# Kernel optimization log

Measured on AMD Instinct MI355X. Metric: run time of the kernel, lower is better.

Reference implementation:

```python
import jax, jax.numpy as jnp
import numpy as np

DIM = 512
NUM_HEADS = 8
HEAD_DIM = DIM // NUM_HEADS
SCALE = HEAD_DIM ** -0.5


def setup_inputs() -> dict:
    key = jax.random.key(0)
    ks = jax.random.split(key, 6)
    B, N, C = 2, 4096, DIM
    s = C ** -0.5  # init scale, torch Linear default-ish
    return {
        "x": jax.random.normal(ks[0], (B, N, C), dtype=jnp.float32),
        "Wq": jax.random.normal(ks[1], (C, C), dtype=jnp.float32) * s,
        "Wk": jax.random.normal(ks[2], (C, C), dtype=jnp.float32) * s,
        "Wv": jax.random.normal(ks[3], (C, C), dtype=jnp.float32) * s,
        "Wo": jax.random.normal(ks[4], (C, C), dtype=jnp.float32) * s,
        "bo": jax.random.normal(ks[5], (C,), dtype=jnp.float32) * s,
    }


def reference(x, Wq, Wk, Wv, Wo, bo):
    B, N, C = x.shape
    H, D = NUM_HEADS, HEAD_DIM
    # torch nn.Linear: y = x @ W.T
    q = (x @ Wq.T).reshape(B, N, H, D).transpose(0, 2, 1, 3)  # [B,H,N,D]
    k = (x @ Wk.T).reshape(B, N, H, D).transpose(0, 2, 1, 3)
    v = (x @ Wv.T).reshape(B, N, H, D).transpose(0, 2, 1, 3)
    attn = jnp.einsum("bhnd,bhmd->bhnm", q, k) * SCALE  # [B,H,N,N]
    attn = jax.nn.softmax(attn, axis=-1)
    out = jnp.einsum("bhnm,bhmd->bhnd", attn, v)
    out = out.transpose(0, 2, 1, 3).reshape(B, N, C)
    return out @ Wo.T + bo
```

## Files before the change

### kernel.cpp

```cpp
#include <hip/hip_runtime.h>
#include <hip/hip_bf16.h>
#include <cstdint>
#include <cstddef>

using bf16 = __bf16;
typedef __attribute__((ext_vector_type(8))) __bf16 bf16x8;
typedef __attribute__((ext_vector_type(4))) float  f32x4;

#define LOG2E 1.4426950408889634f

__device__ inline void gld_lds16(const void* g, void* l) {
  __builtin_amdgcn_global_load_lds(
      (const __attribute__((address_space(1))) void*)g,
      (__attribute__((address_space(3))) void*)l, 16, 0, 0);
}

__global__ __launch_bounds__(256) void k_cvt_all(
    const float* __restrict__ x, const float* __restrict__ wq,
    const float* __restrict__ wk, const float* __restrict__ wv,
    const float* __restrict__ wo, bf16* __restrict__ xb,
    bf16* __restrict__ wqkv, bf16* __restrict__ wob) {
  int i = blockIdx.x * 256 + threadIdx.x;
  const float* s;
  bf16* d;
  int local;
  if (i < 524288) {
    s = x; d = xb; local = i;
  } else {
    int i2 = i - 524288;
    int which = i2 >> 15;
    local = i2 & 32767;
    s = (which == 0) ? wq : (which == 1) ? wk : (which == 2) ? wv : wo;
    d = (which < 3) ? (wqkv + ((size_t)which << 18)) : wob;
  }
  const float4* p = ((const float4*)s) + (size_t)local * 2;
  float4 a = p[0], b = p[1];
  bf16x8 o;
  o[0] = (bf16)a.x; o[1] = (bf16)a.y; o[2] = (bf16)a.z; o[3] = (bf16)a.w;
  o[4] = (bf16)b.x; o[5] = (bf16)b.y; o[6] = (bf16)b.z; o[7] = (bf16)b.w;
  *(bf16x8*)(d + (size_t)local * 8) = o;
}

__global__ __launch_bounds__(256) void k_gemm(
    const bf16* __restrict__ A, const bf16* __restrict__ B, int mode,
    bf16* __restrict__ Qb, bf16* __restrict__ Kb, bf16* __restrict__ Vtb,
    float* __restrict__ outf, const float* __restrict__ bias) {
  const int K = 512;
  __shared__ alignas(16) bf16 As[128 * 64];
  __shared__ alignas(16) bf16 Bs[128 * 64];
  const int tid = threadIdx.x;
  const int wave = tid >> 6, lane = tid & 63;
  const int l15 = lane & 15, l4 = lane >> 4;
  const int m0 = blockIdx.x * 128, n0 = blockIdx.y * 128;
  const int wr = wave >> 1, wc = wave & 1;
  f32x4 acc[4][4] = {};

  for (int k0 = 0; k0 < K; k0 += 64) {
#pragma unroll
    for (int it = 0; it < 4; ++it) {
      int c = it * 256 + tid;
      int row = c >> 3, kc = c & 7;
      int sb = (kc * 16) ^ ((row & 7) << 4);
      gld_lds16((const char*)A + ((size_t)(m0 + row) * K + k0) * 2 + sb,
                (char*)As + c * 16);
      gld_lds16((const char*)B + ((size_t)(n0 + row) * K + k0) * 2 + sb,
                (char*)Bs + c * 16);
    }
    __syncthreads();
#pragma unroll
    for (int ks = 0; ks < 2; ++ks) {
      bf16x8 af[4], bff[4];
#pragma unroll
      for (int mf = 0; mf < 4; ++mf) {
        int r = wr * 64 + mf * 16 + l15;
        af[mf] = *(const bf16x8*)((const char*)As + r * 128 +
                                  ((ks * 64 + l4 * 16) ^ ((r & 7) << 4)));
      }
#pragma unroll
      for (int nf = 0; nf < 4; ++nf) {
        int r = wc * 64 + nf * 16 + l15;
        bff[nf] = *(const bf16x8*)((const char*)Bs + r * 128 +
                                   ((ks * 64 + l4 * 16) ^ ((r & 7) << 4)));
      }
#pragma unroll
      for (int mf = 0; mf < 4; ++mf)
#pragma unroll
        for (int nf = 0; nf < 4; ++nf)
          acc[mf][nf] = __builtin_amdgcn_mfma_f32_16x16x32_bf16(
              af[mf], bff[nf], acc[mf][nf], 0, 0, 0);
    }
    __syncthreads();
  }

#pragma unroll
  for (int mf = 0; mf < 4; ++mf)
#pragma unroll
    for (int nf = 0; nf < 4; ++nf)
#pragma unroll
      for (int r = 0; r < 4; ++r) {
        int m = m0 + wr * 64 + mf * 16 + l4 * 4 + r;
        int n = n0 + wc * 64 + nf * 16 + l15;
        float v = acc[mf][nf][r];
        if (mode == 1) {
          outf[(size_t)m * 512 + n] = v + bias[n];
        } else {
          int which = n >> 9, o = n & 511, h = o >> 6, d = o & 63;
          int b = m >> 12, nr = m & 4095;
          if (which == 0)
            Qb[((size_t)(b * 8 + h) * 4096 + nr) * 64 + d] = (bf16)(v * 0.125f);
          else if (which == 1)
            Kb[((size_t)(b * 8 + h) * 4096 + nr) * 64 + d] = (bf16)v;
          else
            Vtb[((size_t)((b * 8 + h) * 64 + d)) * 4096 + nr] = (bf16)v;
        }
      }
}

template <int NS>
__global__ __launch_bounds__(256, 4) void k_attn_t(
    const bf16* __restrict__ Q, const bf16* __restrict__ Kg,
    const bf16* __restrict__ Vt, bf16* __restrict__ AO,
    float* __restrict__ pO, float* __restrict__ pD) {
  __shared__ alignas(16) bf16 Ks[64 * 64];
  __shared__ alignas(16) bf16 Vs[64 * 64];
  __shared__ alignas(16) bf16 Ps[4][32 * 64];
  const int tid = threadIdx.x, wave = tid >> 6, lane = tid & 63;
  const int l15 = lane & 15, l4 = lane >> 4;
  const int bh = blockIdx.y, q0 = blockIdx.x * 128;
  const int z = (NS > 1) ? blockIdx.z : 0;
  const int n_lo = z * (4096 / NS);
  const int NT = 4096 / NS / 64;
  const char* Qb = (const char*)(Q + (size_t)bh * 4096 * 64);
  const char* Kb = (const char*)(Kg + (size_t)bh * 4096 * 64);
  const char* Vb = (const char*)(Vt + (size_t)bh * 64 * 4096);

  const int c0 = tid, c1 = 256 + tid;
  const int row0 = c0 >> 3, sb0 = ((c0 & 7) * 16) ^ ((row0 & 7) << 4);
  const int row1 = c1 >> 3, sb1 = ((c1 & 7) * 16) ^ ((row1 & 7) << 4);
  const char* ksrc0 = Kb + (size_t)(n_lo + row0) * 128 + sb0;
  const char* ksrc1 = Kb + (size_t)(n_lo + row1) * 128 + sb1;
  const char* vsrc0 = Vb + (size_t)row0 * 8192 + (size_t)n_lo * 2 + sb0;
  const char* vsrc1 = Vb + (size_t)row1 * 8192 + (size_t)n_lo * 2 + sb1;
  char* kdst0 = (char*)Ks + c0 * 16;
  char* kdst1 = (char*)Ks + c1 * 16;
  char* vdst0 = (char*)Vs + c0 * 16;
  char* vdst1 = (char*)Vs + c1 * 16;

  const char* kf_p[2][4];
#pragma unroll
  for (int cf = 0; cf < 4; ++cf) {
    int kv = cf * 16 + l15;
#pragma unroll
    for (int ds = 0; ds < 2; ++ds)
      kf_p[ds][cf] = (const char*)Ks + kv * 128 +
                     ((ds * 64 + l4 * 16) ^ ((kv & 7) << 4));
  }
  const char* vf_p[4][2];
#pragma unroll
  for (int df = 0; df < 4; ++df) {
    int d = df * 16 + l15;
#pragma unroll
    for (int ks = 0; ks < 2; ++ks)
      vf_p[df][ks] = (const char*)Vs + d * 128 +
                     ((ks * 64 + l4 * 16) ^ ((d & 7) << 4));
  }
  char* pw_p[4][4];
#pragma unroll
  for (int r = 0; r < 4; ++r) {
    int q = l4 * 4 + r;
#pragma unroll
    for (int cf = 0; cf < 4; ++cf)
      pw_p[r][cf] = (char*)Ps[wave] + q * 128 +
                    (((cf * 16 + l15) * 2) ^ ((q & 7) << 4));
  }
  const char* pf_p[2];
#pragma unroll
  for (int ks = 0; ks < 2; ++ks)
    pf_p[ks] = (const char*)Ps[wave] + l15 * 128 +
               ((ks * 64 + l4 * 16) ^ ((l15 & 7) << 4));

  bf16x8 qf[2][2];
#pragma unroll
  for (int mrow = 0; mrow < 2; ++mrow)
#pragma unroll
    for (int ds = 0; ds < 2; ++ds)
      qf[mrow][ds] = *(const bf16x8*)(Qb +
          ((size_t)(q0 + wave * 32 + mrow * 16 + l15) * 64 + ds * 32 + l4 * 8) * 2);

  bf16x8 vone;
#pragma unroll
  for (int j = 0; j < 8; ++j) vone[j] = (bf16)1.0f;

  f32x4 oacc[2][4] = {};
  f32x4 dacc[2] = {};

  for (int t = 0; t < NT; ++t) {
    gld_lds16(ksrc0, kdst0);
    gld_lds16(vsrc0, vdst0);
    gld_lds16(ksrc1, kdst1);
    gld_lds16(vsrc1, vdst1);
    ksrc0 += 8192; ksrc1 += 8192;
    vsrc0 += 128;  vsrc1 += 128;
    __syncthreads();

    f32x4 s[2][4];
#pragma unroll
    for (int cf = 0; cf < 4; ++cf) {
      bf16x8 kf0 = *(const bf16x8*)kf_p[0][cf];
      bf16x8 kf1 = *(const bf16x8*)kf_p[1][cf];
#pragma unroll
      for (int mrow = 0; mrow < 2; ++mrow) {
        f32x4 z2 = {};
        z2 = __builtin_amdgcn_mfma_f32_16x16x32_bf16(qf[mrow][0], kf0, z2, 0, 0, 0);
        z2 = __builtin_amdgcn_mfma_f32_16x16x32_bf16(qf[mrow][1], kf1, z2, 0, 0, 0);
        s[mrow][cf] = z2;
      }
    }

#pragma unroll
    for (int mrow = 0; mrow < 2; ++mrow)
#pragma unroll
      for (int r = 0; r < 4; ++r)
#pragma unroll
        for (int cf = 0; cf < 4; ++cf) {
          float p = __builtin_amdgcn_exp2f(s[mrow][cf][r] * LOG2E);
          *(bf16*)(pw_p[r][cf] + mrow * 2048) = (bf16)p;
        }

    bf16x8 pf[2][2];
#pragma unroll
    for (int mrow = 0; mrow < 2; ++mrow) {
      pf[mrow][0] = *(const bf16x8*)(pf_p[0] + mrow * 2048);
      pf[mrow][1] = *(const bf16x8*)(pf_p[1] + mrow * 2048);
    }

#pragma unroll
    for (int mrow = 0; mrow < 2; ++mrow) {
      dacc[mrow] = __builtin_amdgcn_mfma_f32_16x16x32_bf16(pf[mrow][0], vone,
                                                           dacc[mrow], 0, 0, 0);
      dacc[mrow] = __builtin_amdgcn_mfma_f32_16x16x32_bf16(pf[mrow][1], vone,
                                                           dacc[mrow], 0, 0, 0);
    }

#pragma unroll
    for (int df = 0; df < 4; ++df) {
      bf16x8 vf0 = *(const bf16x8*)vf_p[df][0];
      bf16x8 vf1 = *(const bf16x8*)vf_p[df][1];
#pragma unroll
      for (int mrow = 0; mrow < 2; ++mrow) {
        oacc[mrow][df] = __builtin_amdgcn_mfma_f32_16x16x32_bf16(
            pf[mrow][0], vf0, oacc[mrow][df], 0, 0, 0);
        oacc[mrow][df] = __builtin_amdgcn_mfma_f32_16x16x32_bf16(
            pf[mrow][1], vf1, oacc[mrow][df], 0, 0, 0);
      }
    }
    __syncthreads();
  }

  if (NS > 1) {
    float* po = pO + (((size_t)(z * 16 + bh)) * 4096) * 64;
    float* pd = pD + ((size_t)(z * 16 + bh)) * 4096;
#pragma unroll
    for (int mrow = 0; mrow < 2; ++mrow)
#pragma unroll
      for (int r = 0; r < 4; ++r) {
        int n = q0 + wave * 32 + mrow * 16 + l4 * 4 + r;
#pragma unroll
        for (int df = 0; df < 4; ++df)
          po[(size_t)n * 64 + df * 16 + l15] = oacc[mrow][df][r];
        if (l15 == 0) pd[n] = dacc[mrow][r];
      }
  } else {
    int b = bh >> 3, h = bh & 7;
#pragma unroll
    for (int mrow = 0; mrow < 2; ++mrow)
#pragma unroll
      for (int r = 0; r < 4; ++r) {
        float inv = 1.0f / dacc[mrow][r];
        int n = q0 + wave * 32 + mrow * 16 + l4 * 4 + r;
#pragma unroll
        for (int df = 0; df < 4; ++df) {
          int d = df * 16 + l15;
          AO[((size_t)(b * 4096 + n)) * 512 + h * 64 + d] =
              (bf16)(oacc[mrow][df][r] * inv);
        }
      }
  }
}

__global__ __launch_bounds__(256) void k_comb(
    const float* __restrict__ pO, const float* __restrict__ pD,
    bf16* __restrict__ AO) {
  const size_t SO = (size_t)16 * 4096 * 64;
  const size_t SD = (size_t)16 * 4096;
  int i = blockIdx.x * 256 + threadIdx.x;
  int g = i >> 3, j = i & 7;
  float den = pD[g] + pD[g + SD];
  float inv = 1.0f / den;
  const float* a = pO + (size_t)g * 64 + j * 8;
  const float* b2 = a + SO;
  bf16x8 o;
#pragma unroll
  for (int t = 0; t < 8; ++t) o[t] = (bf16)((a[t] + b2[t]) * inv);
  int bh = g >> 12, n = g & 4095, b = bh >> 3, h = bh & 7;
  *(bf16x8*)(AO + ((size_t)(b * 4096 + n)) * 512 + h * 64 + j * 8) = o;
}

extern "C" void kernel_launch(void* const* d_in, const int* in_sizes, int n_in,
                              void* d_out, int out_size, void* d_ws,
                              size_t ws_size, hipStream_t stream) {
  const float* x  = (const float*)d_in[0];
  const float* Wq = (const float*)d_in[1];
  const float* Wk = (const float*)d_in[2];
  const float* Wv = (const float*)d_in[3];
  const float* Wo = (const float*)d_in[4];
  const float* bo = (const float*)d_in[5];
  float* out = (float*)d_out;

  char* ws = (char*)d_ws;
  bf16* xb   = (bf16*)(ws);
  bf16* wqkv = (bf16*)(ws + (8u << 20));
  bf16* wob  = (bf16*)(ws + (8u << 20) + 1572864u);
  bf16* Qb   = (bf16*)(ws + (10u << 20));
  bf16* Kb   = (bf16*)(ws + (18u << 20));
  bf16* Vtb  = (bf16*)(ws + (26u << 20));
  bf16* AOb  = (bf16*)(ws + (34u << 20));
  float* pD  = (float*)(ws + (42u << 20));
  float* pO  = (float*)(ws + (43u << 20));

  k_cvt_all<<<2560, 256, 0, stream>>>(x, Wq, Wk, Wv, Wo, xb, wqkv, wob);

  k_gemm<<<dim3(64, 12), 256, 0, stream>>>(xb, wqkv, 0, Qb, Kb, Vtb,
                                           nullptr, nullptr);

  if (ws_size >= ((size_t)75 << 20)) {
    k_attn_t<2><<<dim3(32, 16, 2), 256, 0, stream>>>(Qb, Kb, Vtb, nullptr,
                                                     pO, pD);
    k_comb<<<2048, 256, 0, stream>>>(pO, pD, AOb);
  } else {
    k_attn_t<1><<<dim3(32, 16), 256, 0, stream>>>(Qb, Kb, Vtb, AOb,
                                                  nullptr, nullptr);
  }

  k_gemm<<<dim3(64, 4), 256, 0, stream>>>(AOb, wob, 1, nullptr, nullptr,
                                          nullptr, out, bo);
}
```

Measured before the change: 161.2 us.

## Double-buffer K/V LDS tiles in attention kernel to overlap loads with compute

Doubles the shared-memory K and V tiles and restructures the attention loop into a ping-pong pipeline. The next tile's global-to-LDS loads are issued before computing on the current buffer. The aim is to hide global load latency behind the MFMA and exp work. In exchange, LDS use per block rises from about 32KB to 48KB, which may lower occupancy at 4 blocks per CU. The code also assumes NT is even, and the loop relies on the barrier placement to keep the ping-pong buffers correct.

```diff
diff --git a/kernel.cpp b/kernel.cpp
--- a/kernel.cpp
+++ b/kernel.cpp
@@ -121,8 +121,8 @@
     const bf16* __restrict__ Q, const bf16* __restrict__ Kg,
     const bf16* __restrict__ Vt, bf16* __restrict__ AO,
     float* __restrict__ pO, float* __restrict__ pD) {
-  __shared__ alignas(16) bf16 Ks[64 * 64];
-  __shared__ alignas(16) bf16 Vs[64 * 64];
+  __shared__ alignas(16) bf16 Ks[2][64 * 64];
+  __shared__ alignas(16) bf16 Vs[2][64 * 64];
   __shared__ alignas(16) bf16 Ps[4][32 * 64];
   const int tid = threadIdx.x, wave = tid >> 6, lane = tid & 63;
   const int l15 = lane & 15, l4 = lane >> 4;
@@ -194,68 +194,83 @@
   f32x4 oacc[2][4] = {};
   f32x4 dacc[2] = {};
 
-  for (int t = 0; t < NT; ++t) {
-    gld_lds16(ksrc0, kdst0);
-    gld_lds16(vsrc0, vdst0);
-    gld_lds16(ksrc1, kdst1);
-    gld_lds16(vsrc1, vdst1);
-    ksrc0 += 8192; ksrc1 += 8192;
-    vsrc0 += 128;  vsrc1 += 128;
+#define STAGE(BO)                                                             \
+  do {                                                                        \
+    gld_lds16(ksrc0, kdst0 + (BO));                                           \
+    gld_lds16(vsrc0, vdst0 + (BO));                                           \
+    gld_lds16(ksrc1, kdst1 + (BO));                                           \
+    gld_lds16(vsrc1, vdst1 + (BO));                                           \
+    ksrc0 += 8192; ksrc1 += 8192;                                             \
+    vsrc0 += 128;  vsrc1 += 128;                                              \
+  } while (0)
+
+#define COMPUTE(BO)                                                           \
+  do {                                                                        \
+    f32x4 s[2][4];                                                            \
+    _Pragma("unroll")                                                         \
+    for (int cf = 0; cf < 4; ++cf) {                                          \
+      bf16x8 kf0 = *(const bf16x8*)(kf_p[0][cf] + (BO));                      \
+      bf16x8 kf1 = *(const bf16x8*)(kf_p[1][cf] + (BO));                      \
+      _Pragma("unroll")                                                       \
+      for (int mrow = 0; mrow < 2; ++mrow) {                                  \
+        f32x4 z2 = {};                                                        \
+        z2 = __builtin_amdgcn_mfma_f32_16x16x32_bf16(qf[mrow][0], kf0, z2,    \
+                                                     0, 0, 0);                \
+        z2 = __builtin_amdgcn_mfma_f32_16x16x32_bf16(qf[mrow][1], kf1, z2,    \
+                                                     0, 0, 0);                \
+        s[mrow][cf] = z2;                                                     \
+      }                                                                       \
+    }                                                                         \
+    _Pragma("unroll")                                                         \
+    for (int mrow = 0; mrow < 2; ++mrow)                                      \
+      _Pragma("unroll")                                                       \
+      for (int r = 0; r < 4; ++r)                                             \
+        _Pragma("unroll")                                                     \
+        for (int cf = 0; cf < 4; ++cf) {                                      \
+          float p = __builtin_amdgcn_exp2f(s[mrow][cf][r] * LOG2E);           \
+          *(bf16*)(pw_p[r][cf] + mrow * 2048) = (bf16)p;                      \
+        }                                                                     \
+    bf16x8 pf[2][2];                                                          \
+    _Pragma("unroll")                                                         \
+    for (int mrow = 0; mrow < 2; ++mrow) {                                    \
+      pf[mrow][0] = *(const bf16x8*)(pf_p[0] + mrow * 2048);                  \
+      pf[mrow][1] = *(const bf16x8*)(pf_p[1] + mrow * 2048);                  \
+    }                                                                         \
+    _Pragma("unroll")                                                         \
+    for (int mrow = 0; mrow < 2; ++mrow) {                                    \
+      dacc[mrow] = __builtin_amdgcn_mfma_f32_16x16x32_bf16(                   \
+          pf[mrow][0], vone, dacc[mrow], 0, 0, 0);                            \
+      dacc[mrow] = __builtin_amdgcn_mfma_f32_16x16x32_bf16(                   \
+          pf[mrow][1], vone, dacc[mrow], 0, 0, 0);                            \
+    }                                                                         \
+    _Pragma("unroll")                                                         \
+    for (int df = 0; df < 4; ++df) {                                          \
+      bf16x8 vf0 = *(const bf16x8*)(vf_p[df][0] + (BO));                      \
+      bf16x8 vf1 = *(const bf16x8*)(vf_p[df][1] + (BO));                      \
+      _Pragma("unroll")                                                       \
+      for (int mrow = 0; mrow < 2; ++mrow) {                                  \
+        oacc[mrow][df] = __builtin_amdgcn_mfma_f32_16x16x32_bf16(             \
+            pf[mrow][0], vf0, oacc[mrow][df], 0, 0, 0);                       \
+        oacc[mrow][df] = __builtin_amdgcn_mfma_f32_16x16x32_bf16(             \
+            pf[mrow][1], vf1, oacc[mrow][df], 0, 0, 0);                       \
+      }                                                                       \
+    }                                                                         \
+  } while (0)
+
+  STAGE(0);
+  __syncthreads();
+
+  const int NP = NT / 2;
+  for (int p = 0; p < NP; ++p) {
+    STAGE(8192);
+    COMPUTE(0);
     __syncthreads();
-
-    f32x4 s[2][4];
-#pragma unroll
-    for (int cf = 0; cf < 4; ++cf) {
-      bf16x8 kf0 = *(const bf16x8*)kf_p[0][cf];
-      bf16x8 kf1 = *(const bf16x8*)kf_p[1][cf];
-#pragma unroll
-      for (int mrow = 0; mrow < 2; ++mrow) {
-        f32x4 z2 = {};
-        z2 = __builtin_amdgcn_mfma_f32_16x16x32_bf16(qf[mrow][0], kf0, z2, 0, 0, 0);
-        z2 = __builtin_amdgcn_mfma_f32_16x16x32_bf16(qf[mrow][1], kf1, z2, 0, 0, 0);
-        s[mrow][cf] = z2;
-      }
-    }
-
-#pragma unroll
-    for (int mrow = 0; mrow < 2; ++mrow)
-#pragma unroll
-      for (int r = 0; r < 4; ++r)
-#pragma unroll
-        for (int cf = 0; cf < 4; ++cf) {
-          float p = __builtin_amdgcn_exp2f(s[mrow][cf][r] * LOG2E);
-          *(bf16*)(pw_p[r][cf] + mrow * 2048) = (bf16)p;
-        }
-
-    bf16x8 pf[2][2];
-#pragma unroll
-    for (int mrow = 0; mrow < 2; ++mrow) {
-      pf[mrow][0] = *(const bf16x8*)(pf_p[0] + mrow * 2048);
-      pf[mrow][1] = *(const bf16x8*)(pf_p[1] + mrow * 2048);
-    }
-
-#pragma unroll
-    for (int mrow = 0; mrow < 2; ++mrow) {
-      dacc[mrow] = __builtin_amdgcn_mfma_f32_16x16x32_bf16(pf[mrow][0], vone,
-                                                           dacc[mrow], 0, 0, 0);
-      dacc[mrow] = __builtin_amdgcn_mfma_f32_16x16x32_bf16(pf[mrow][1], vone,
-                                                           dacc[mrow], 0, 0, 0);
-    }
-
-#pragma unroll
-    for (int df = 0; df < 4; ++df) {
-      bf16x8 vf0 = *(const bf16x8*)vf_p[df][0];
-      bf16x8 vf1 = *(const bf16x8*)vf_p[df][1];
-#pragma unroll
-      for (int mrow = 0; mrow < 2; ++mrow) {
-        oacc[mrow][df] = __builtin_amdgcn_mfma_f32_16x16x32_bf16(
-            pf[mrow][0], vf0, oacc[mrow][df], 0, 0, 0);
-        oacc[mrow][df] = __builtin_amdgcn_mfma_f32_16x16x32_bf16(
-            pf[mrow][1], vf1, oacc[mrow][df], 0, 0, 0);
-      }
-    }
+    if (p + 1 < NP) STAGE(0);
+    COMPUTE(8192);
     __syncthreads();
   }
+#undef STAGE
+#undef COMPUTE
 
   if (NS > 1) {
     float* po = pO + (((size_t)(z * 16 + bh)) * 4096) * 64;
```

Measured after the change: 178.3 us. 10.6% more time.
